# Kernel optimization log

Hardware: AMD Instinct MI355X
Metric: run time of the kernel (lower is better)

Reference implementation:

```python
import jax, jax.numpy as jnp
import numpy as np

N_DRUG = 572
EMB = 512
K_NB = 64
SEG_NB = 16
BN_EPS = 1e-5


def setup_inputs() -> dict:
    key = jax.random.key(0)
    ks = jax.random.split(key, 8)
    return {
        "drug_name": jnp.arange(N_DRUG, dtype=jnp.int64) if jax.config.jax_enable_x64 else jnp.arange(N_DRUG, dtype=jnp.int32),
        "adj_tail": jax.random.randint(ks[0], (N_DRUG, K_NB), 0, 100000),
        "adj_relation": jax.random.randint(ks[1], (N_DRUG, K_NB), 0, 200),
        "inv_adj_idx": jax.random.randint(ks[2], (N_DRUG, SEG_NB), 0, N_DRUG),
        "drug_table": jax.random.normal(ks[3], (N_DRUG, EMB), dtype=jnp.float32),
        "rela_table": jax.random.normal(ks[4], (200, EMB), dtype=jnp.float32),
        "ent_table": jax.random.normal(ks[5], (100000, EMB), dtype=jnp.float32),
        "W_lin": jax.random.normal(ks[6], (2 * EMB, EMB), dtype=jnp.float32) * (1.0 / np.sqrt(2 * EMB)),
        "b_lin": jnp.zeros((EMB,), jnp.float32),
        "bn_gamma": jnp.ones((EMB,), jnp.float32),
        "bn_beta": jnp.zeros((EMB,), jnp.float32),
        "epoch": 2,
    }


def _forward(drug_name, adj_tail, adj_relation, inv_adj_idx,
             drug_table, rela_table, ent_table, W_lin, b_lin,
             bn_gamma, bn_beta, epoch):
    # Embedding gathers
    drug_emb = drug_table[drug_name]          # [N, D]
    rel_emb = rela_table[adj_relation]        # [N, K, D]
    ent_emb = ent_table[adj_tail]             # [N, K, D]

    # KGCN-style attention over sampled neighbors: score_k = softmax(drug . rel_k)
    scores = jax.nn.softmax(jnp.einsum('nd,nkd->nk', drug_emb, rel_emb), axis=1)
    attended = jnp.einsum('nk,nkd->nd', scores, ent_emb)  # [N, D]

    # Linear -> ReLU -> BatchNorm1d (training-mode batch stats, biased var)
    e = jnp.concatenate([attended, drug_emb], axis=1)     # [N, 2D]
    h = jax.nn.relu(e @ W_lin + b_lin)                    # [N, D]
    mu = jnp.mean(h, axis=0)
    var = jnp.mean(jnp.square(h - mu), axis=0)
    drug_f = bn_gamma * (h - mu) * jax.lax.rsqrt(var + BN_EPS) + bn_beta

    if epoch > 1:
        # Sequential in-place neighbor averaging (faithful to the Python loop:
        # later drugs see already-updated rows).
        def body(f, x):
            i, pos = x
            avg = jnp.mean(f[pos], axis=0)                # [D]
            f = f.at[i].set((avg + f[i]) * 0.5)
            return f, None
        idxs = jnp.arange(N_DRUG)
        drug_f, _ = jax.lax.scan(body, drug_f, (idxs, inv_adj_idx))
    return drug_f


def reference(drug_name, adj_tail, adj_relation, inv_adj_idx,
              drug_table, rela_table, ent_table, W_lin, b_lin,
              bn_gamma, bn_beta, epoch):
    return _forward(drug_name, adj_tail, adj_relation, inv_adj_idx,
                    drug_table, rela_table, ent_table, W_lin, b_lin,
                    bn_gamma, bn_beta, epoch)
```

## Files before the change

### kernel.cpp

```cpp
#include <hip/hip_runtime.h>
#include <hip/hip_bf16.h>

#define N_DRUG 572
#define EMB    512
#define K_NB   64
#define SEG_NB 16
#define SCOLS  16

typedef __hip_bfloat16  bf16;
typedef __hip_bfloat162 bf162;

__device__ __forceinline__ float b2f(bf16 x){ return __bfloat162float(x); }

template<typename T> __device__ __forceinline__ float ldf(const T* p);
template<> __device__ __forceinline__ float ldf<float>(const float* p){ return *p; }
template<> __device__ __forceinline__ float ldf<bf16>(const bf16* p){ return b2f(*p); }

template<typename T> __device__ __forceinline__ float2 ld2(const T* p);
template<> __device__ __forceinline__ float2 ld2<float>(const float* p){ return *(const float2*)p; }
template<> __device__ __forceinline__ float2 ld2<bf16>(const bf16* p){
    bf162 v = *(const bf162*)p; return make_float2(b2f(v.x), b2f(v.y));
}

template<typename T> __device__ __forceinline__ void st2(T* p, float x, float y);
template<> __device__ __forceinline__ void st2<float>(float* p, float x, float y){ *(float2*)p = make_float2(x, y); }
template<> __device__ __forceinline__ void st2<bf16>(bf16* p, float x, float y){
    bf162 v; v.x = __float2bfloat16(x); v.y = __float2bfloat16(y); *(bf162*)p = v;
}

__device__ __forceinline__ bool idx_is64(const void* drug_name) {
    return ((const int*)drug_name)[1] == 0;
}
__device__ __forceinline__ int ld_idx(const void* p, int i, bool is64) {
    return is64 ? (int)((const long long*)p)[i] : ((const int*)p)[i];
}

__device__ __forceinline__ bool detect_bf16(const void* tab) {
    const int lane = threadIdx.x & 63;
    int hit = 0;
    if (lane < 32) {
        const unsigned u = ((const unsigned*)tab)[lane * 997];
        const unsigned e = (u >> 7) & 0xffu;
        hit = (e >= 110u && e <= 141u) ? 1 : 0;
    }
    return __popcll(__ballot(hit)) >= 24;
}

struct __align__(16) FwdSmem {
    float e[2][2 * EMB];
    float sc[2][K_NB];
    int   tl[2][K_NB];
};

template<typename T>
__device__ void fwd_impl(FwdSmem& sm,
    const void* drug_name, const void* adj_tail, const void* adj_rel,
    const T* __restrict__ drug_table, const T* __restrict__ rela_table,
    const T* __restrict__ ent_table,  const T* __restrict__ W,
    const T* __restrict__ bl, T* __restrict__ h)
{
    const int  t    = threadIdx.x;
    const int  n0   = blockIdx.x * 2;
    const bool is64 = idx_is64(drug_name);

    #pragma unroll
    for (int dr = 0; dr < 2; ++dr) {
        const int row = ld_idx(drug_name, n0 + dr, is64);
        const float2 v = ld2(drug_table + (size_t)row * EMB + 2 * t);
        sm.e[dr][EMB + 2 * t]     = v.x;
        sm.e[dr][EMB + 2 * t + 1] = v.y;
    }
    if (t < 128) {
        const int dr = t >> 6, k = t & 63;
        sm.tl[dr][k] = ld_idx(adj_tail, (n0 + dr) * K_NB + k, is64);
    }
    __syncthreads();

    {
        const int wave = t >> 6, lane = t & 63;
        const int dr = wave >> 1;
        const int kb = (wave & 1) * 32;
        const float* ed = &sm.e[dr][EMB];
        #pragma unroll 4
        for (int i = 0; i < 32; ++i) {
            const int k   = kb + i;
            const int rid = ld_idx(adj_rel, (n0 + dr) * K_NB + k, is64);
            const T* rl = rela_table + (size_t)rid * EMB;
            float p = 0.f;
            #pragma unroll
            for (int m = 0; m < 4; ++m) {
                const int dd = 2 * lane + m * 128;
                const float2 rv = ld2(rl + dd);
                p = fmaf(ed[dd],     rv.x, p);
                p = fmaf(ed[dd + 1], rv.y, p);
            }
            #pragma unroll
            for (int off = 32; off; off >>= 1) p += __shfl_down(p, off, 64);
            if (lane == 0) sm.sc[dr][k] = p;
        }
    }
    __syncthreads();

    if (t < 128) {
        const int dr = t >> 6, k = t & 63;
        const float s = sm.sc[dr][k];
        float m = s;
        #pragma unroll
        for (int off = 32; off; off >>= 1) m = fmaxf(m, __shfl_xor(m, off, 64));
        const float ex = __expf(s - m);
        float sum = ex;
        #pragma unroll
        for (int off = 32; off; off >>= 1) sum += __shfl_xor(sum, off, 64);
        sm.sc[dr][k] = ex / sum;
    }
    __syncthreads();

    {
        float a00 = 0.f, a01 = 0.f, a10 = 0.f, a11 = 0.f;
        #pragma unroll 4
        for (int k = 0; k < K_NB; ++k) {
            const float w0 = sm.sc[0][k], w1 = sm.sc[1][k];
            const float2 v0 = ld2(ent_table + (size_t)sm.tl[0][k] * EMB + 2 * t);
            const float2 v1 = ld2(ent_table + (size_t)sm.tl[1][k] * EMB + 2 * t);
            a00 = fmaf(w0, v0.x, a00); a01 = fmaf(w0, v0.y, a01);
            a10 = fmaf(w1, v1.x, a10); a11 = fmaf(w1, v1.y, a11);
        }
        sm.e[0][2 * t] = a00; sm.e[0][2 * t + 1] = a01;
        sm.e[1][2 * t] = a10; sm.e[1][2 * t + 1] = a11;
    }
    __syncthreads();

    {
        const int d0 = 2 * t;
        const float2 bb = ld2(bl + d0);
        float a00 = bb.x, a01 = bb.y, a10 = bb.x, a11 = bb.y;
        const float4* E0 = (const float4*)&sm.e[0][0];
        const float4* E1 = (const float4*)&sm.e[1][0];
        #pragma unroll 2
        for (int q = 0; q < (2 * EMB) / 4; ++q) {
            const float4 f0 = E0[q];
            const float4 f1 = E1[q];
            const T* Wp = W + (size_t)(4 * q) * EMB + d0;
            const float2 w0 = ld2(Wp);
            const float2 w1 = ld2(Wp + EMB);
            const float2 w2 = ld2(Wp + 2 * EMB);
            const float2 w3 = ld2(Wp + 3 * EMB);
            a00 = fmaf(f0.x, w0.x, a00); a01 = fmaf(f0.x, w0.y, a01);
            a10 = fmaf(f1.x, w0.x, a10); a11 = fmaf(f1.x, w0.y, a11);
            a00 = fmaf(f0.y, w1.x, a00); a01 = fmaf(f0.y, w1.y, a01);
            a10 = fmaf(f1.y, w1.x, a10); a11 = fmaf(f1.y, w1.y, a11);
            a00 = fmaf(f0.z, w2.x, a00); a01 = fmaf(f0.z, w2.y, a01);
            a10 = fmaf(f1.z, w2.x, a10); a11 = fmaf(f1.z, w2.y, a11);
            a00 = fmaf(f0.w, w3.x, a00); a01 = fmaf(f0.w, w3.y, a01);
            a10 = fmaf(f1.w, w3.x, a10); a11 = fmaf(f1.w, w3.y, a11);
        }
        st2(h + (size_t)n0 * EMB + d0,       fmaxf(a00, 0.f), fmaxf(a01, 0.f));
        st2(h + (size_t)(n0 + 1) * EMB + d0, fmaxf(a10, 0.f), fmaxf(a11, 0.f));
    }
}

__global__ __launch_bounds__(256) void k_fwd(
    const void* drug_name, const void* adj_tail, const void* adj_rel,
    const void* drug_tab, const void* rela_tab, const void* ent_tab,
    const void* W, const void* bl, void* h)
{
    __shared__ FwdSmem sm;
    if (detect_bf16(drug_tab))
        fwd_impl<bf16>(sm, drug_name, adj_tail, adj_rel,
                       (const bf16*)drug_tab, (const bf16*)rela_tab,
                       (const bf16*)ent_tab, (const bf16*)W,
                       (const bf16*)bl, (bf16*)h);
    else
        fwd_impl<float>(sm, drug_name, adj_tail, adj_rel,
                        (const float*)drug_tab, (const float*)rela_tab,
                        (const float*)ent_tab, (const float*)W,
                        (const float*)bl, (float*)h);
}

struct __align__(16) ScanSmem {
    float    fbuf[N_DRUG * SCOLS];
    unsigned obuf[N_DRUG * SEG_NB];
    float2   corr[576];
};

__device__ __forceinline__ float bflo(unsigned u){ return __uint_as_float(u << 16); }
__device__ __forceinline__ float bfhi(unsigned u){ return __uint_as_float(u & 0xffff0000u); }
__device__ __forceinline__ unsigned pack_bf2(float a, float b) {
    bf162 v; v.x = __float2bfloat16(a); v.y = __float2bfloat16(b);
    unsigned u; __builtin_memcpy(&u, &v, 4); return u;
}

template<typename T>
__device__ __forceinline__ void stage_fbuf(float* fbuf, const T* h, int c0, int t);
template<>
__device__ __forceinline__ void stage_fbuf<float>(float* fbuf, const float* h, int c0, int t) {
    float4* dst = (float4*)fbuf;
    #pragma unroll 4
    for (int k = t; k < N_DRUG * 4; k += 64)
        dst[k] = *(const float4*)(h + (size_t)(k >> 2) * EMB + c0 + 4 * (k & 3));
}
template<>
__device__ __forceinline__ void stage_fbuf<bf16>(float* fbuf, const bf16* h, int c0, int t) {
    float4* dst = (float4*)fbuf;
    #pragma unroll 4
    for (int k = t; k < N_DRUG * 2; k += 64) {
        const uint4 v = *(const uint4*)(h + (size_t)(k >> 1) * EMB + c0 + 8 * (k & 1));
        dst[2 * k]     = make_float4(bflo(v.x), bfhi(v.x), bflo(v.y), bfhi(v.y));
        dst[2 * k + 1] = make_float4(bflo(v.z), bfhi(v.z), bflo(v.w), bfhi(v.w));
    }
}

template<typename T>
__device__ __forceinline__ void flush_fbuf(const float* fbuf, T* h, int c0, int t);
template<>
__device__ __forceinline__ void flush_fbuf<float>(const float* fbuf, float* h, int c0, int t) {
    const float4* src = (const float4*)fbuf;
    #pragma unroll 4
    for (int k = t; k < N_DRUG * 4; k += 64)
        *(float4*)(h + (size_t)(k >> 2) * EMB + c0 + 4 * (k & 3)) = src[k];
}
template<>
__device__ __forceinline__ void flush_fbuf<bf16>(const float* fbuf, bf16* h, int c0, int t) {
    const float4* src = (const float4*)fbuf;
    #pragma unroll 4
    for (int k = t; k < N_DRUG * 2; k += 64) {
        const float4 f0 = src[2 * k], f1 = src[2 * k + 1];
        uint4 o;
        o.x = pack_bf2(f0.x, f0.y); o.y = pack_bf2(f0.z, f0.w);
        o.z = pack_bf2(f1.x, f1.y); o.w = pack_bf2(f1.z, f1.w);
        *(uint4*)(h + (size_t)(k >> 1) * EMB + c0 + 8 * (k & 1)) = o;
    }
}

template<bool IS64>
__device__ __forceinline__ void stage_obuf(unsigned* obuf, const void* inv, int t) {
    const uint4* src = (const uint4*)inv;
    if (IS64) {
        #pragma unroll 4
        for (int k = t; k < (N_DRUG * SEG_NB) / 2; k += 64) {
            const uint4 v = src[k];
            *(uint2*)(obuf + 2 * k) = make_uint2(v.x << 4, v.z << 4);
        }
    } else {
        uint4* dst = (uint4*)obuf;
        #pragma unroll 4
        for (int k = t; k < (N_DRUG * SEG_NB) / 4; k += 64) {
            uint4 v = src[k];
            v.x <<= 4; v.y <<= 4; v.z <<= 4; v.w <<= 4;
            dst[k] = v;
        }
    }
}

#define BODY(Vc, Vn, Qn, Fc, Cc, I)                                          \
    {                                                                        \
        Vn.x = fb[Qn.x + c]; Vn.y = fb[Qn.y + c];                            \
        Vn.z = fb[Qn.z + c]; Vn.w = fb[Qn.w + c];                            \
        Qn = ob4[(((I) + 6 <= N_DRUG - 1) ? (I) + 6 : N_DRUG - 1) * 4 + g];  \
        float s = (Vc.x + Vc.y) + (Vc.z + Vc.w);                             \
        s += __shfl_xor(s, 16, 64);                                          \
        s += __shfl_xor(s, 32, 64);                                          \
        float nv = fmaf(s, 1.f / 32.f, Fc * 0.5f);                           \
        nv = fmaf(Cc.x, nv1 - f1, nv);                                       \
        nv = fmaf(Cc.y, nv2 - f2, nv);                                       \
        f2 = f1; f1 = Fc; nv2 = nv1; nv1 = nv;                               \
        Fc = fb[(((I) + 4 <= N_DRUG - 1) ? (I) + 4 : N_DRUG - 1) * 16 + c];  \
        Cc = sm.corr[(I) + 4];                                               \
        if (g == 0) sm.fbuf[(I) * SCOLS + c] = nv;                           \
    }

template<typename T, bool IS64>
__device__ void scan_impl(ScanSmem& sm, T* __restrict__ h,
    const void* __restrict__ inv, const T* __restrict__ gamma,
    const T* __restrict__ beta, const void* __restrict__ epoch)
{
    const int t  = threadIdx.x;
    const int c0 = blockIdx.x * SCOLS;

    stage_obuf<IS64>(sm.obuf, inv, t);
    stage_fbuf<T>(sm.fbuf, h, c0, t);
    for (int k = t; k < 576; k += 64) sm.corr[k] = make_float2(0.f, 0.f);
    __syncthreads();

    for (int i = 1 + t; i < N_DRUG; i += 64) {
        const unsigned tA = (unsigned)(i - 1) << 4;
        const unsigned tB = (unsigned)(i - 2) << 4;
        int cA = 0, cB = 0;
        #pragma unroll
        for (int j = 0; j < SEG_NB; ++j) {
            const unsigned o = sm.obuf[i * SEG_NB + j];
            cA += (o == tA) ? 1 : 0;
            cB += (o == tB) ? 1 : 0;
        }
        sm.corr[i] = make_float2((float)cA * (1.f / 32.f), (float)cB * (1.f / 32.f));
    }

    {
        const int c = t & 15, g = t >> 4;
        float s = 0.f, s2 = 0.f;
        for (int r = g; r < N_DRUG; r += 4) {
            const float x = sm.fbuf[r * SCOLS + c];
            s += x; s2 = fmaf(x, x, s2);
        }
        s  += __shfl_xor(s, 16, 64);  s  += __shfl_xor(s, 32, 64);
        s2 += __shfl_xor(s2, 16, 64); s2 += __shfl_xor(s2, 32, 64);
        const float mu  = s * (1.f / N_DRUG);
        const float var = fmaxf(s2 * (1.f / N_DRUG) - mu * mu, 0.f);
        const float gs  = ldf(gamma + c0 + c) * rsqrtf(var + 1e-5f);
        const float bs  = ldf(beta  + c0 + c);
        for (int r = g; r < N_DRUG; r += 4) {
            const float x = sm.fbuf[r * SCOLS + c];
            sm.fbuf[r * SCOLS + c] = fmaf(x - mu, gs, bs);
        }
    }
    __syncthreads();

    if (((const int*)epoch)[0] > 1) {
        const int c = t & 15, g = t >> 4;
        const float* fb  = sm.fbuf;
        const uint4* ob4 = (const uint4*)sm.obuf;

        float4 V0, V1, V2{}, V3{};
        uint4  Q0, Q1, Q2, Q3;
        float  F0, F1, F2, F3;
        float2 C0, C1, C2, C3;

        {
            const uint4 o0 = ob4[0 * 4 + g], o1 = ob4[1 * 4 + g];
            V0.x = fb[o0.x + c]; V0.y = fb[o0.y + c];
            V0.z = fb[o0.z + c]; V0.w = fb[o0.w + c];
            V1.x = fb[o1.x + c]; V1.y = fb[o1.y + c];
            V1.z = fb[o1.z + c]; V1.w = fb[o1.w + c];
            Q2 = ob4[2 * 4 + g]; Q3 = ob4[3 * 4 + g];
            Q0 = ob4[4 * 4 + g]; Q1 = ob4[5 * 4 + g];
            F0 = fb[0 * 16 + c]; F1 = fb[1 * 16 + c];
            F2 = fb[2 * 16 + c]; F3 = fb[3 * 16 + c];
            C0 = sm.corr[0]; C1 = sm.corr[1];
            C2 = sm.corr[2]; C3 = sm.corr[3];
        }
        float nv1 = 0.f, nv2 = 0.f, f1 = 0.f, f2 = 0.f;

        for (int i = 0; i < N_DRUG; i += 4) {
            BODY(V0, V2, Q2, F0, C0, i);
            BODY(V1, V3, Q3, F1, C1, i + 1);
            BODY(V2, V0, Q0, F2, C2, i + 2);
            BODY(V3, V1, Q1, F3, C3, i + 3);
        }
    }
    __syncthreads();

    flush_fbuf<T>(sm.fbuf, h, c0, t);
}

__global__ __launch_bounds__(64) void k_scan(
    void* h, const void* inv, const void* gamma, const void* beta,
    const void* epoch, const void* drug_name, const void* drug_tab)
{
    __shared__ ScanSmem sm;
    const bool isbf = detect_bf16(drug_tab);
    const bool is64 = idx_is64(drug_name);
    if (isbf) {
        if (is64) scan_impl<bf16, true >(sm, (bf16*)h, inv, (const bf16*)gamma, (const bf16*)beta, epoch);
        else      scan_impl<bf16, false>(sm, (bf16*)h, inv, (const bf16*)gamma, (const bf16*)beta, epoch);
    } else {
        if (is64) scan_impl<float, true >(sm, (float*)h, inv, (const float*)gamma, (const float*)beta, epoch);
        else      scan_impl<float, false>(sm, (float*)h, inv, (const float*)gamma, (const float*)beta, epoch);
    }
}

extern "C" void kernel_launch(void* const* d_in, const int* in_sizes, int n_in,
                              void* d_out, int out_size, void* d_ws, size_t ws_size,
                              hipStream_t stream)
{
    (void)in_sizes; (void)n_in; (void)out_size; (void)d_ws; (void)ws_size;

    k_fwd<<<N_DRUG / 2, 256, 0, stream>>>(
        d_in[0], d_in[1], d_in[2],
        d_in[4], d_in[5], d_in[6],
        d_in[7], d_in[8],
        d_out);
    k_scan<<<EMB / SCOLS, 64, 0, stream>>>(
        d_out, d_in[3],
        d_in[9], d_in[10], d_in[11],
        d_in[0], d_in[4]);
}
```

Before: 442.7 us.

## Process four drugs per block and deepen scan gather pipeline

The forward kernel now handles four drugs per block instead of two. That halves the number of W_lin reads per drug and stages relation indices in shared memory. Relation scores now use 16-lane subgroups, so four neighbours are scored per wave pass. The sequential scan keeps three prior-step corrections instead of two, so gathered neighbour sums can be issued one step further ahead and taken off the serial dependency chain. The trade-off is fewer blocks (143) for the forward pass and more registers and correction terms in the scan.

```diff
diff --git a/kernel.cpp b/kernel.cpp
--- a/kernel.cpp
+++ b/kernel.cpp
@@ -6,6 +6,7 @@
 #define K_NB   64
 #define SEG_NB 16
 #define SCOLS  16
+#define DPB    4
 
 typedef __hip_bfloat16  bf16;
 typedef __hip_bfloat162 bf162;
@@ -47,9 +48,10 @@
 }
 
 struct __align__(16) FwdSmem {
-    float e[2][2 * EMB];
-    float sc[2][K_NB];
-    int   tl[2][K_NB];
+    float e[DPB][2 * EMB];
+    float sc[DPB][K_NB];
+    int   tl[DPB][K_NB];
+    int   rl[DPB][K_NB];
 };
 
 template<typename T>
@@ -60,48 +62,50 @@
     const T* __restrict__ bl, T* __restrict__ h)
 {
     const int  t    = threadIdx.x;
-    const int  n0   = blockIdx.x * 2;
+    const int  n0   = blockIdx.x * DPB;
     const bool is64 = idx_is64(drug_name);
 
     #pragma unroll
-    for (int dr = 0; dr < 2; ++dr) {
+    for (int dr = 0; dr < DPB; ++dr) {
         const int row = ld_idx(drug_name, n0 + dr, is64);
         const float2 v = ld2(drug_table + (size_t)row * EMB + 2 * t);
         sm.e[dr][EMB + 2 * t]     = v.x;
         sm.e[dr][EMB + 2 * t + 1] = v.y;
     }
-    if (t < 128) {
+    {
         const int dr = t >> 6, k = t & 63;
-        sm.tl[dr][k] = ld_idx(adj_tail, (n0 + dr) * K_NB + k, is64);
+        sm.tl[dr][k] = ld_idx(adj_tail, n0 * K_NB + t, is64);
+        sm.rl[dr][k] = ld_idx(adj_rel,  n0 * K_NB + t, is64);
     }
     __syncthreads();
 
     {
         const int wave = t >> 6, lane = t & 63;
-        const int dr = wave >> 1;
-        const int kb = (wave & 1) * 32;
-        const float* ed = &sm.e[dr][EMB];
-        #pragma unroll 4
-        for (int i = 0; i < 32; ++i) {
-            const int k   = kb + i;
-            const int rid = ld_idx(adj_rel, (n0 + dr) * K_NB + k, is64);
-            const T* rl = rela_table + (size_t)rid * EMB;
+        const int g = lane >> 4, c = lane & 15;
+        const float* ed = &sm.e[wave][EMB];
+        #pragma unroll 2
+        for (int pass = 0; pass < 16; ++pass) {
+            const int k = pass * 4 + g;
+            const T* rl = rela_table + (size_t)sm.rl[wave][k] * EMB;
             float p = 0.f;
             #pragma unroll
-            for (int m = 0; m < 4; ++m) {
-                const int dd = 2 * lane + m * 128;
+            for (int m = 0; m < 16; ++m) {
+                const int dd = 2 * c + 32 * m;
                 const float2 rv = ld2(rl + dd);
-                p = fmaf(ed[dd],     rv.x, p);
-                p = fmaf(ed[dd + 1], rv.y, p);
+                const float2 ev = *(const float2*)&ed[dd];
+                p = fmaf(ev.x, rv.x, p);
+                p = fmaf(ev.y, rv.y, p);
             }
-            #pragma unroll
-            for (int off = 32; off; off >>= 1) p += __shfl_down(p, off, 64);
-            if (lane == 0) sm.sc[dr][k] = p;
-        }
-    }
-    __syncthreads();
-
-    if (t < 128) {
+            p += __shfl_xor(p, 1, 64);
+            p += __shfl_xor(p, 2, 64);
+            p += __shfl_xor(p, 4, 64);
+            p += __shfl_xor(p, 8, 64);
+            if (c == 0) sm.sc[wave][k] = p;
+        }
+    }
+    __syncthreads();
+
+    {
         const int dr = t >> 6, k = t & 63;
         const float s = sm.sc[dr][k];
         float m = s;
@@ -116,46 +120,53 @@
     __syncthreads();
 
     {
-        float a00 = 0.f, a01 = 0.f, a10 = 0.f, a11 = 0.f;
-        #pragma unroll 4
+        float a0[DPB], a1[DPB];
+        #pragma unroll
+        for (int dr = 0; dr < DPB; ++dr) { a0[dr] = 0.f; a1[dr] = 0.f; }
+        #pragma unroll 2
         for (int k = 0; k < K_NB; ++k) {
-            const float w0 = sm.sc[0][k], w1 = sm.sc[1][k];
-            const float2 v0 = ld2(ent_table + (size_t)sm.tl[0][k] * EMB + 2 * t);
-            const float2 v1 = ld2(ent_table + (size_t)sm.tl[1][k] * EMB + 2 * t);
-            a00 = fmaf(w0, v0.x, a00); a01 = fmaf(w0, v0.y, a01);
-            a10 = fmaf(w1, v1.x, a10); a11 = fmaf(w1, v1.y, a11);
-        }
-        sm.e[0][2 * t] = a00; sm.e[0][2 * t + 1] = a01;
-        sm.e[1][2 * t] = a10; sm.e[1][2 * t + 1] = a11;
+            #pragma unroll
+            for (int dr = 0; dr < DPB; ++dr) {
+                const float w  = sm.sc[dr][k];
+                const float2 v = ld2(ent_table + (size_t)sm.tl[dr][k] * EMB + 2 * t);
+                a0[dr] = fmaf(w, v.x, a0[dr]);
+                a1[dr] = fmaf(w, v.y, a1[dr]);
+            }
+        }
+        #pragma unroll
+        for (int dr = 0; dr < DPB; ++dr) {
+            sm.e[dr][2 * t]     = a0[dr];
+            sm.e[dr][2 * t + 1] = a1[dr];
+        }
     }
     __syncthreads();
 
     {
         const int d0 = 2 * t;
         const float2 bb = ld2(bl + d0);
-        float a00 = bb.x, a01 = bb.y, a10 = bb.x, a11 = bb.y;
-        const float4* E0 = (const float4*)&sm.e[0][0];
-        const float4* E1 = (const float4*)&sm.e[1][0];
+        float a0[DPB], a1[DPB];
+        #pragma unroll
+        for (int dr = 0; dr < DPB; ++dr) { a0[dr] = bb.x; a1[dr] = bb.y; }
         #pragma unroll 2
         for (int q = 0; q < (2 * EMB) / 4; ++q) {
-            const float4 f0 = E0[q];
-            const float4 f1 = E1[q];
             const T* Wp = W + (size_t)(4 * q) * EMB + d0;
             const float2 w0 = ld2(Wp);
             const float2 w1 = ld2(Wp + EMB);
             const float2 w2 = ld2(Wp + 2 * EMB);
             const float2 w3 = ld2(Wp + 3 * EMB);
-            a00 = fmaf(f0.x, w0.x, a00); a01 = fmaf(f0.x, w0.y, a01);
-            a10 = fmaf(f1.x, w0.x, a10); a11 = fmaf(f1.x, w0.y, a11);
-            a00 = fmaf(f0.y, w1.x, a00); a01 = fmaf(f0.y, w1.y, a01);
-            a10 = fmaf(f1.y, w1.x, a10); a11 = fmaf(f1.y, w1.y, a11);
-            a00 = fmaf(f0.z, w2.x, a00); a01 = fmaf(f0.z, w2.y, a01);
-            a10 = fmaf(f1.z, w2.x, a10); a11 = fmaf(f1.z, w2.y, a11);
-            a00 = fmaf(f0.w, w3.x, a00); a01 = fmaf(f0.w, w3.y, a01);
-            a10 = fmaf(f1.w, w3.x, a10); a11 = fmaf(f1.w, w3.y, a11);
-        }
-        st2(h + (size_t)n0 * EMB + d0,       fmaxf(a00, 0.f), fmaxf(a01, 0.f));
-        st2(h + (size_t)(n0 + 1) * EMB + d0, fmaxf(a10, 0.f), fmaxf(a11, 0.f));
+            #pragma unroll
+            for (int dr = 0; dr < DPB; ++dr) {
+                const float4 f = ((const float4*)&sm.e[dr][0])[q];
+                a0[dr] = fmaf(f.x, w0.x, a0[dr]); a1[dr] = fmaf(f.x, w0.y, a1[dr]);
+                a0[dr] = fmaf(f.y, w1.x, a0[dr]); a1[dr] = fmaf(f.y, w1.y, a1[dr]);
+                a0[dr] = fmaf(f.z, w2.x, a0[dr]); a1[dr] = fmaf(f.z, w2.y, a1[dr]);
+                a0[dr] = fmaf(f.w, w3.x, a0[dr]); a1[dr] = fmaf(f.w, w3.y, a1[dr]);
+            }
+        }
+        #pragma unroll
+        for (int dr = 0; dr < DPB; ++dr)
+            st2(h + (size_t)(n0 + dr) * EMB + d0,
+                fmaxf(a0[dr], 0.f), fmaxf(a1[dr], 0.f));
     }
 }
 
@@ -180,7 +191,7 @@
 struct __align__(16) ScanSmem {
     float    fbuf[N_DRUG * SCOLS];
     unsigned obuf[N_DRUG * SEG_NB];
-    float2   corr[576];
+    float4   corr[576];
 };
 
 __device__ __forceinline__ float bflo(unsigned u){ return __uint_as_float(u << 16); }
@@ -252,21 +263,24 @@
     }
 }
 
-#define BODY(Vc, Vn, Qn, Fc, Cc, I)                                          \
+#define RMIN(X) (((X) < N_DRUG) ? (X) : (N_DRUG - 1))
+
+#define BODY4(Vg, Qg, Sc, Fc, Cc, Vr, Sr, I)                                 \
     {                                                                        \
-        Vn.x = fb[Qn.x + c]; Vn.y = fb[Qn.y + c];                            \
-        Vn.z = fb[Qn.z + c]; Vn.w = fb[Qn.w + c];                            \
-        Qn = ob4[(((I) + 6 <= N_DRUG - 1) ? (I) + 6 : N_DRUG - 1) * 4 + g];  \
-        float s = (Vc.x + Vc.y) + (Vc.z + Vc.w);                             \
-        s += __shfl_xor(s, 16, 64);                                          \
-        s += __shfl_xor(s, 32, 64);                                          \
-        float nv = fmaf(s, 1.f / 32.f, Fc * 0.5f);                           \
+        Vg.x = fb[Qg.x + c]; Vg.y = fb[Qg.y + c];                            \
+        Vg.z = fb[Qg.z + c]; Vg.w = fb[Qg.w + c];                            \
+        Qg = ob4[RMIN((I) + 7) * 4 + g];                                     \
+        float nv = fmaf(Sc, 1.f / 32.f, Fc * 0.5f);                          \
         nv = fmaf(Cc.x, nv1 - f1, nv);                                       \
         nv = fmaf(Cc.y, nv2 - f2, nv);                                       \
-        f2 = f1; f1 = Fc; nv2 = nv1; nv1 = nv;                               \
-        Fc = fb[(((I) + 4 <= N_DRUG - 1) ? (I) + 4 : N_DRUG - 1) * 16 + c];  \
+        nv = fmaf(Cc.z, nv3 - f3, nv);                                       \
+        f3 = f2; f2 = f1; f1 = Fc; nv3 = nv2; nv2 = nv1; nv1 = nv;           \
+        if (g == 0) sm.fbuf[(I) * SCOLS + c] = nv;                           \
+        Fc = fb[RMIN((I) + 4) * 16 + c];                                     \
         Cc = sm.corr[(I) + 4];                                               \
-        if (g == 0) sm.fbuf[(I) * SCOLS + c] = nv;                           \
+        float l = (Vr.x + Vr.y) + (Vr.z + Vr.w);                             \
+        Sr = (l + __shfl_xor(l, 16, 64)) +                                   \
+             (__shfl_xor(l, 32, 64) + __shfl_xor(l, 48, 64));                \
     }
 
 template<typename T, bool IS64>
@@ -279,20 +293,24 @@
 
     stage_obuf<IS64>(sm.obuf, inv, t);
     stage_fbuf<T>(sm.fbuf, h, c0, t);
-    for (int k = t; k < 576; k += 64) sm.corr[k] = make_float2(0.f, 0.f);
+    for (int k = t; k < 576; k += 64) sm.corr[k] = make_float4(0.f, 0.f, 0.f, 0.f);
     __syncthreads();
 
     for (int i = 1 + t; i < N_DRUG; i += 64) {
         const unsigned tA = (unsigned)(i - 1) << 4;
         const unsigned tB = (unsigned)(i - 2) << 4;
-        int cA = 0, cB = 0;
+        const unsigned tC = (unsigned)(i - 3) << 4;
+        int cA = 0, cB = 0, cC = 0;
         #pragma unroll
         for (int j = 0; j < SEG_NB; ++j) {
             const unsigned o = sm.obuf[i * SEG_NB + j];
             cA += (o == tA) ? 1 : 0;
             cB += (o == tB) ? 1 : 0;
-        }
-        sm.corr[i] = make_float2((float)cA * (1.f / 32.f), (float)cB * (1.f / 32.f));
+            cC += (o == tC) ? 1 : 0;
+        }
+        sm.corr[i] = make_float4((float)cA * (1.f / 32.f),
+                                 (float)cB * (1.f / 32.f),
+                                 (float)cC * (1.f / 32.f), 0.f);
     }
 
     {
@@ -320,31 +338,40 @@
         const float* fb  = sm.fbuf;
         const uint4* ob4 = (const uint4*)sm.obuf;
 
-        float4 V0, V1, V2{}, V3{};
+        float4 V0, V1, V2, V3;
         uint4  Q0, Q1, Q2, Q3;
-        float  F0, F1, F2, F3;
-        float2 C0, C1, C2, C3;
 
         {
-            const uint4 o0 = ob4[0 * 4 + g], o1 = ob4[1 * 4 + g];
+            const uint4 o0 = ob4[0 * 4 + g], o1 = ob4[1 * 4 + g], o2 = ob4[2 * 4 + g];
             V0.x = fb[o0.x + c]; V0.y = fb[o0.y + c];
             V0.z = fb[o0.z + c]; V0.w = fb[o0.w + c];
             V1.x = fb[o1.x + c]; V1.y = fb[o1.y + c];
             V1.z = fb[o1.z + c]; V1.w = fb[o1.w + c];
-            Q2 = ob4[2 * 4 + g]; Q3 = ob4[3 * 4 + g];
-            Q0 = ob4[4 * 4 + g]; Q1 = ob4[5 * 4 + g];
-            F0 = fb[0 * 16 + c]; F1 = fb[1 * 16 + c];
-            F2 = fb[2 * 16 + c]; F3 = fb[3 * 16 + c];
-            C0 = sm.corr[0]; C1 = sm.corr[1];
-            C2 = sm.corr[2]; C3 = sm.corr[3];
-        }
-        float nv1 = 0.f, nv2 = 0.f, f1 = 0.f, f2 = 0.f;
+            V2.x = fb[o2.x + c]; V2.y = fb[o2.y + c];
+            V2.z = fb[o2.z + c]; V2.w = fb[o2.w + c];
+        }
+        Q3 = ob4[3 * 4 + g];
+        Q0 = ob4[4 * 4 + g]; Q1 = ob4[5 * 4 + g]; Q2 = ob4[6 * 4 + g];
+        float F0 = fb[0 * 16 + c], F1 = fb[1 * 16 + c];
+        float F2 = fb[2 * 16 + c], F3 = fb[3 * 16 + c];
+        float4 C0 = sm.corr[0], C1 = sm.corr[1];
+        float4 C2 = sm.corr[2], C3 = sm.corr[3];
+        float S0, S1, S2 = 0.f, S3 = 0.f;
+        {
+            float l0 = (V0.x + V0.y) + (V0.z + V0.w);
+            S0 = (l0 + __shfl_xor(l0, 16, 64)) +
+                 (__shfl_xor(l0, 32, 64) + __shfl_xor(l0, 48, 64));
+            float l1 = (V1.x + V1.y) + (V1.z + V1.w);
+            S1 = (l1 + __shfl_xor(l1, 16, 64)) +
+                 (__shfl_xor(l1, 32, 64) + __shfl_xor(l1, 48, 64));
+        }
+        float nv1 = 0.f, nv2 = 0.f, nv3 = 0.f, f1 = 0.f, f2 = 0.f, f3 = 0.f;
 
         for (int i = 0; i < N_DRUG; i += 4) {
-            BODY(V0, V2, Q2, F0, C0, i);
-            BODY(V1, V3, Q3, F1, C1, i + 1);
-            BODY(V2, V0, Q0, F2, C2, i + 2);
-            BODY(V3, V1, Q1, F3, C3, i + 3);
+            BODY4(V3, Q3, S0, F0, C0, V2, S2, i);
+            BODY4(V0, Q0, S1, F1, C1, V3, S3, i + 1);
+            BODY4(V1, Q1, S2, F2, C2, V0, S0, i + 2);
+            BODY4(V2, Q2, S3, F3, C3, V1, S1, i + 3);
         }
     }
     __syncthreads();
@@ -374,7 +401,7 @@
 {
     (void)in_sizes; (void)n_in; (void)out_size; (void)d_ws; (void)ws_size;
 
-    k_fwd<<<N_DRUG / 2, 256, 0, stream>>>(
+    k_fwd<<<N_DRUG / DPB, 256, 0, stream>>>(
         d_in[0], d_in[1], d_in[2],
         d_in[4], d_in[5], d_in[6],
         d_in[7], d_in[8],
```

Result: no change. 442.1 us (-0.1%).
